# Kernel optimization log

Hardware: AMD Instinct MI355X
Metric: run time of the kernel (lower is better)

## Reference

```python
import jax, jax.numpy as jnp
import numpy as np

CORR_RADIUS = 4  # matches init corr_radius


def setup_inputs() -> dict:
    key = jax.random.key(0)
    k1, k2 = jax.random.split(key)
    B, C, H, W = 8, 256, 96, 128
    x1 = jax.random.normal(k1, (B, C, H, W), dtype=jnp.float32)
    x2 = jax.random.normal(k2, (B, C, H, W), dtype=jnp.float32)
    return {"x1": x1, "x2": x2}


def reference(x1, x2):
    # Local cost volume: for each of the (2r+1)^2 displacements, the
    # unfolded tensor that the torch version builds.
    B, C, H, W = x1.shape
    r = CORR_RADIUS
    D = 2 * r + 1
    x2p = jnp.pad(x2, ((0, 0), (0, 0), (r, r), (r, r)))  # [B,C,H+2r,W+2r]
    inv_c = jnp.asarray(1.0 / C, dtype=x1.dtype)
    outs = []
    for di in range(D):          # small fixed displacement set (9x9)
        for dj in range(D):
            shifted = x2p[:, :, di:di + H, dj:dj + W]  # [B,C,H,W]
            outs.append(jnp.einsum('bchw,bchw->bhw', x1, shifted) * inv_c)
    # torch ordering: unfold over H first then W -> row-major over (di,dj)
    return jnp.stack(outs, axis=1)  # [B, D*D, H, W]
```

## Files before the change

kernel.cpp:

```cpp
#include <hip/hip_runtime.h>

#define Cc 256
#define Hh 96
#define Ww 128
#define CH_STRIDE (Hh * Ww)
#define ROWS 16
#define SCOLS 24
#define ACOLS 32
#define CSL  48

typedef __attribute__((ext_vector_type(8))) short bf16x8;
typedef __attribute__((ext_vector_type(4))) float f32x4;

static __device__ __forceinline__ unsigned cvt_pk(float lo, float hi) {
  unsigned r;
  asm("v_cvt_pk_bf16_f32 %0, %1, %2" : "=v"(r) : "v"(lo), "v"(hi));
  return r;
}

#define FCOMP(v, cc) ((cc) == 0 ? (v).x : (cc) == 1 ? (v).y : (cc) == 2 ? (v).z : (v).w)

#define PF_LOAD(pf, cx)                                               \
  do {                                                                \
    const size_t cb_ = (size_t)(cx) * 32 * CH_STRIDE;                 \
    _Pragma("unroll")                                                 \
    for (int j = 0; j < 8; ++j)                                       \
      pf[j] = sok ? *(const float4*)(sptr + cb_ + (size_t)j * CH_STRIDE) \
                  : make_float4(0.f, 0.f, 0.f, 0.f);                  \
  } while (0)

#define LDS_WRITE(pf)                                                 \
  do {                                                                \
    _Pragma("unroll")                                                 \
    for (int cc = 0; cc < 4; ++cc) {                                  \
      uint4 pk;                                                       \
      pk.x = cvt_pk(FCOMP(pf[0], cc), FCOMP(pf[1], cc));              \
      pk.y = cvt_pk(FCOMP(pf[2], cc), FCOMP(pf[3], cc));              \
      pk.z = cvt_pk(FCOMP(pf[4], cc), FCOMP(pf[5], cc));              \
      pk.w = cvt_pk(FCOMP(pf[6], cc), FCOMP(pf[7], cc));              \
      *(uint4*)(&x2s[soff + cc * CSL]) = pk;                          \
    }                                                                 \
  } while (0)

__global__ __launch_bounds__(512)
void corr_mfma(const float* __restrict__ x1, const float* __restrict__ x2,
               float* __restrict__ out) {
  __shared__ __align__(16) unsigned short x2s[ROWS * ACOLS * CSL];

  const int tid  = threadIdx.x;
  const int bid  = blockIdx.x;
  const int sbid = (bid & 7) * 96 + (bid >> 3);

  const int wt  = sbid & 7;
  const int hgb = sbid >> 3;
  const int hg  = hgb % 12;
  const int b   = hgb / 12;
  const int h0  = hg * 8;
  const int w0  = wt * 16;

  const int wv   = tid >> 6;
  const int lane = tid & 63;
  const int n16  = lane & 15;
  const int kgrp = lane >> 4;
  const int h    = h0 + wv;

  const bool stager = (tid < 384);
  const int ug   = tid % 6;
  const int ur   = (tid / 6) % 16;
  const int uchg = tid / 96;
  const int gh   = h0 - 4 + ur;
  const int gw0  = w0 - 4 + 4 * ug;
  const bool sok = stager & (gh >= 0) & (gh < Hh) & (gw0 >= 0) & (gw0 + 3 < Ww);
  const int ghc  = sok ? gh : 0;
  const int gwc  = sok ? gw0 : 0;
  const float* sptr = x2 + ((size_t)(b * Cc + uchg * 8) * Hh + ghc) * Ww + gwc;
  const int soff = (ur * ACOLS + 4 * ug) * CSL + (((uchg + ur) & 3) << 3);

  const float* pA = x1 + ((size_t)b * Cc * Hh + h) * Ww + (w0 + n16)
                       + (size_t)kgrp * 8 * CH_STRIDE;

  f32x4 acc[9][2];
#pragma unroll
  for (int di = 0; di < 9; ++di)
#pragma unroll
    for (int t = 0; t < 2; ++t) acc[di][t] = (f32x4){0.f, 0.f, 0.f, 0.f};

  float4 pf[8];
  if (stager) PF_LOAD(pf, 0);

  for (int ci = 0; ci < 8; ++ci) {
    __syncthreads();

    float pa[8];
    {
      const float* pAc = pA + (size_t)(ci * 32) * CH_STRIDE;
#pragma unroll
      for (int j = 0; j < 8; ++j) pa[j] = pAc[(size_t)j * CH_STRIDE];
    }

    if (stager) LDS_WRITE(pf);

    bf16x8 af;
    {
      union { unsigned u[4]; bf16x8 v; } ux;
      ux.u[0] = cvt_pk(pa[0], pa[1]);
      ux.u[1] = cvt_pk(pa[2], pa[3]);
      ux.u[2] = cvt_pk(pa[4], pa[5]);
      ux.u[3] = cvt_pk(pa[6], pa[7]);
      af = ux.v;
    }

    if (stager && ci < 7) PF_LOAD(pf, ci + 1);

    __syncthreads();

#pragma unroll
    for (int di = 0; di < 9; ++di) {
      const int r_ = wv + di;
      const int slot = ((kgrp + r_) & 3) << 3;
#pragma unroll
      for (int t = 0; t < 2; ++t) {
        const bf16x8 bf_ =
            *(const bf16x8*)(&x2s[(r_ * ACOLS + 16 * t + n16) * CSL + slot]);
        acc[di][t] = __builtin_amdgcn_mfma_f32_16x16x32_bf16(af, bf_, acc[di][t], 0, 0, 0);
      }
    }
  }

  const float scale = 1.0f / (float)Cc;
#pragma unroll
  for (int di = 0; di < 9; ++di) {
#pragma unroll
    for (int t = 0; t < 2; ++t) {
#pragma unroll
      for (int q = 0; q < 4; ++q) {
        const int m  = kgrp * 4 + q;
        const int dj = 16 * t + n16 - m;
        if (dj >= 0 && dj <= 8) {
          out[(((size_t)b * 81 + di * 9 + dj) * Hh + h) * Ww + (w0 + m)]
              = acc[di][t][q] * scale;
        }
      }
    }
  }
}

extern "C" void kernel_launch(void* const* d_in, const int* in_sizes, int n_in,
                              void* d_out, int out_size, void* d_ws, size_t ws_size,
                              hipStream_t stream) {
  const float* x1 = (const float*)d_in[0];
  const float* x2 = (const float*)d_in[1];
  float* out = (float*)d_out;
  corr_mfma<<<768, 512, 0, stream>>>(x1, x2, out);
}
```

Before: 62.69 us.

## Double-buffer x2 LDS tile and compact row layout with new swizzle

Switches the x2 staging buffer in LDS to two buffers, so the next channel chunk is written while MFMAs read the current one. This cuts the two barriers per iteration to one. The row stride shrinks from 32 to 24 cells and uses a new column-based swizzle (CPHYS) in place of the row/channel-group slot rotation, so two buffers fit in LDS. The cost is doubled LDS use per block, which may reduce occupancy, and the new swizzle may change the pattern of bank conflicts.

```diff
diff --git a/kernel.cpp b/kernel.cpp
--- a/kernel.cpp
+++ b/kernel.cpp
@@ -6,11 +6,14 @@
 #define CH_STRIDE (Hh * Ww)
 #define ROWS 16
 #define SCOLS 24
-#define ACOLS 32
 #define CSL  48
+#define CELLS_PER_ROW 24
+#define BUF_SHORTS 19200
 
 typedef __attribute__((ext_vector_type(8))) short bf16x8;
 typedef __attribute__((ext_vector_type(4))) float f32x4;
+
+#define CPHYS(c) (((c) & ~3) | (((c) + ((c) >> 2)) & 3))
 
 static __device__ __forceinline__ unsigned cvt_pk(float lo, float hi) {
   unsigned r;
@@ -29,7 +32,7 @@
                   : make_float4(0.f, 0.f, 0.f, 0.f);                  \
   } while (0)
 
-#define LDS_WRITE(pf)                                                 \
+#define LDS_WRITE(pf, bs)                                             \
   do {                                                                \
     _Pragma("unroll")                                                 \
     for (int cc = 0; cc < 4; ++cc) {                                  \
@@ -38,14 +41,29 @@
       pk.y = cvt_pk(FCOMP(pf[2], cc), FCOMP(pf[3], cc));              \
       pk.z = cvt_pk(FCOMP(pf[4], cc), FCOMP(pf[5], cc));              \
       pk.w = cvt_pk(FCOMP(pf[6], cc), FCOMP(pf[7], cc));              \
-      *(uint4*)(&x2s[soff + cc * CSL]) = pk;                          \
+      *(uint4*)(&x2s[(bs) * BUF_SHORTS + wbase                        \
+                     + CPHYS(4 * ug + cc) * CSL]) = pk;               \
+    }                                                                 \
+  } while (0)
+
+#define COMPUTE(af, bs)                                               \
+  do {                                                                \
+    _Pragma("unroll")                                                 \
+    for (int di = 0; di < 9; ++di) {                                  \
+      const int rb_ = (bs) * BUF_SHORTS + (wv + di) * (CELLS_PER_ROW * CSL); \
+      _Pragma("unroll")                                               \
+      for (int t = 0; t < 2; ++t) {                                   \
+        const bf16x8 bf_ = *(const bf16x8*)(&x2s[rb_ + rd[t]]);       \
+        acc[di][t] = __builtin_amdgcn_mfma_f32_16x16x32_bf16(         \
+            af, bf_, acc[di][t], 0, 0, 0);                            \
+      }                                                               \
     }                                                                 \
   } while (0)
 
 __global__ __launch_bounds__(512)
 void corr_mfma(const float* __restrict__ x1, const float* __restrict__ x2,
                float* __restrict__ out) {
-  __shared__ __align__(16) unsigned short x2s[ROWS * ACOLS * CSL];
+  __shared__ __align__(16) unsigned short x2s[2 * BUF_SHORTS];
 
   const int tid  = threadIdx.x;
   const int bid  = blockIdx.x;
@@ -74,7 +92,14 @@
   const int ghc  = sok ? gh : 0;
   const int gwc  = sok ? gw0 : 0;
   const float* sptr = x2 + ((size_t)(b * Cc + uchg * 8) * Hh + ghc) * Ww + gwc;
-  const int soff = (ur * ACOLS + 4 * ug) * CSL + (((uchg + ur) & 3) << 3);
+  const int wbase = ur * (CELLS_PER_ROW * CSL) + uchg * 8;
+
+  int rd[2];
+#pragma unroll
+  for (int t = 0; t < 2; ++t) {
+    const int col = 16 * t + n16;
+    rd[t] = CPHYS(col) * CSL + kgrp * 8;
+  }
 
   const float* pA = x1 + ((size_t)b * Cc * Hh + h) * Ww + (w0 + n16)
                        + (size_t)kgrp * 8 * CH_STRIDE;
@@ -86,20 +111,21 @@
     for (int t = 0; t < 2; ++t) acc[di][t] = (f32x4){0.f, 0.f, 0.f, 0.f};
 
   float4 pf[8];
-  if (stager) PF_LOAD(pf, 0);
+  if (stager) {
+    PF_LOAD(pf, 0);
+    LDS_WRITE(pf, 0);
+    PF_LOAD(pf, 1);
+  }
+  __syncthreads();
 
   for (int ci = 0; ci < 8; ++ci) {
-    __syncthreads();
-
+    const int bs = ci & 1;
     float pa[8];
     {
       const float* pAc = pA + (size_t)(ci * 32) * CH_STRIDE;
 #pragma unroll
       for (int j = 0; j < 8; ++j) pa[j] = pAc[(size_t)j * CH_STRIDE];
     }
-
-    if (stager) LDS_WRITE(pf);
-
     bf16x8 af;
     {
       union { unsigned u[4]; bf16x8 v; } ux;
@@ -110,21 +136,15 @@
       af = ux.v;
     }
 
-    if (stager && ci < 7) PF_LOAD(pf, ci + 1);
+    COMPUTE(af, bs);
 
-    __syncthreads();
-
-#pragma unroll
-    for (int di = 0; di < 9; ++di) {
-      const int r_ = wv + di;
-      const int slot = ((kgrp + r_) & 3) << 3;
-#pragma unroll
-      for (int t = 0; t < 2; ++t) {
-        const bf16x8 bf_ =
-            *(const bf16x8*)(&x2s[(r_ * ACOLS + 16 * t + n16) * CSL + slot]);
-        acc[di][t] = __builtin_amdgcn_mfma_f32_16x16x32_bf16(af, bf_, acc[di][t], 0, 0, 0);
+    if (ci < 7) {
+      if (stager) {
+        LDS_WRITE(pf, bs ^ 1);
+        if (ci < 6) PF_LOAD(pf, ci + 2);
       }
     }
+    __syncthreads();
   }
 
   const float scale = 1.0f / (float)Cc;
```

Result: slower. 70.12 us (+11.9%).
